# Performance work log

Hardware: AMD Instinct MI355X
Metric: run time of the kernel (lower is better)

The kernel has to match this reference:

```python
import jax, jax.numpy as jnp
import numpy as np

B, C, N = 8, 512, 2048

def setup_inputs() -> dict:
    key = jax.random.key(0)
    ks = jax.random.split(key, 7)
    s = 1.0 / np.sqrt(C)
    return {
        "x": jax.random.normal(ks[0], (B, C, N), dtype=jnp.float32),
        "wq": jax.random.normal(ks[1], (C, C), dtype=jnp.float32) * s,
        "bq": jax.random.normal(ks[2], (C,), dtype=jnp.float32) * s,
        "wk": jax.random.normal(ks[3], (C, C), dtype=jnp.float32) * s,
        "bk": jax.random.normal(ks[4], (C,), dtype=jnp.float32) * s,
        "wv": jax.random.normal(ks[5], (C, C), dtype=jnp.float32) * s,
        "bv": jax.random.normal(ks[6], (C,), dtype=jnp.float32) * s,
    }

def reference(x, wq, bq, wk, bk, wv, bv):
    # Conv1d with kernel=1 == pointwise channel matmul: [B,C,N] -> [B,C,N]
    q = jnp.einsum('oc,bcn->bon', wq, x) + bq[None, :, None]
    k = jnp.einsum('oc,bcn->bon', wk, x) + bk[None, :, None]
    v = jnp.einsum('oc,bcn->bon', wv, x) + bv[None, :, None]
    # scores[b,i,j] = sum_c q[b,c,i] * k[b,c,j]; softmax over j (no scaling, as in source)
    scores = jnp.einsum('bci,bcj->bij', q, k)
    attn = jax.nn.softmax(scores, axis=-1)  # [B,N,N]
    # out[b,c,i] = sum_j v[b,c,j] * attn[b,i,j]
    out = jnp.einsum('bcj,bij->bci', v, attn)
    return out + x
```

## Files before the change

kernel.cpp:

```cpp
#include <hip/hip_runtime.h>
#include <hip/hip_bf16.h>

typedef _Float16 half_t;
typedef _Float16 f16x8 __attribute__((ext_vector_type(8)));
typedef float f32x4 __attribute__((ext_vector_type(4)));

#define AS1 __attribute__((address_space(1)))
#define AS3 __attribute__((address_space(3)))

constexpr int CB = 512;
constexpr int NB = 2048;
constexpr int BB = 8;

__device__ inline f32x4 mfma16(f16x8 a, f16x8 b, f32x4 c) {
  return __builtin_amdgcn_mfma_f32_16x16x32_f16(a, b, c, 0, 0, 0);
}

__global__ void convert_w(const float* __restrict__ wv, half_t* __restrict__ wvh) {
  int i = blockIdx.x * 256 + threadIdx.x;
  if (i < CB * CB) wvh[i] = (half_t)wv[i];
}

__global__ __launch_bounds__(256) void compute_G_part(const float* __restrict__ wq,
                                                      const float* __restrict__ wk,
                                                      float* __restrict__ Gp) {
  __shared__ float aq[64][68];
  __shared__ float ak[64][68];
  const int c0 = blockIdx.y * 64, d0 = blockIdx.x * 64, o0 = blockIdx.z * 64;
  const int t = threadIdx.x;
  {
    const int r = t >> 2, cbase = (t & 3) * 16;
    const float* q = wq + (size_t)(o0 + r) * CB + c0 + cbase;
    const float* k = wk + (size_t)(o0 + r) * CB + d0 + cbase;
#pragma unroll
    for (int q4 = 0; q4 < 4; q4++) {
      *(float4*)&aq[r][cbase + q4 * 4] = *(const float4*)(q + q4 * 4);
      *(float4*)&ak[r][cbase + q4 * 4] = *(const float4*)(k + q4 * 4);
    }
  }
  __syncthreads();
  const int tc = t & 15, td = t >> 4;
  float acc[4][4] = {};
#pragma unroll 8
  for (int o = 0; o < 64; o++) {
    float4 a4 = *(const float4*)&aq[o][tc * 4];
    float4 b4 = *(const float4*)&ak[o][td * 4];
    float av[4] = {a4.x, a4.y, a4.z, a4.w};
    float bv[4] = {b4.x, b4.y, b4.z, b4.w};
#pragma unroll
    for (int i = 0; i < 4; i++)
#pragma unroll
      for (int j = 0; j < 4; j++)
        acc[i][j] += av[i] * bv[j];
  }
  float* gz = Gp + (size_t)blockIdx.z * CB * CB;
#pragma unroll
  for (int i = 0; i < 4; i++) {
    int c = c0 + tc * 4 + i;
#pragma unroll
    for (int j = 0; j < 4; j++)
      gz[(size_t)c * CB + d0 + td * 4 + j] = acc[i][j];
  }
}

__global__ void reduce_G(const float* __restrict__ Gp, half_t* __restrict__ Gh) {
  int i = blockIdx.x * 256 + threadIdx.x;
  if (i >= CB * CB) return;
  float s = 0.0f;
#pragma unroll
  for (int z = 0; z < 8; z++) s += Gp[(size_t)z * CB * CB + i];
  Gh[i] = (half_t)s;
}

__global__ void compute_u(const float* __restrict__ wk, const float* __restrict__ bq,
                          float* __restrict__ u) {
  int d = blockIdx.x * 256 + threadIdx.x;
  if (d >= CB) return;
  float s = 0.0f;
  for (int o = 0; o < CB; o++) s += bq[o] * wk[(size_t)o * CB + d];
  u[d] = s;
}

__global__ __launch_bounds__(256) void compute_ubias(const half_t* __restrict__ xh,
                                                     const float* __restrict__ u,
                                                     float* __restrict__ ub) {
  __shared__ float us[CB];
  for (int i = threadIdx.x; i < CB; i += 256) us[i] = u[i];
  __syncthreads();
  int row = blockIdx.x * 4 + (threadIdx.x >> 6);
  int lane = threadIdx.x & 63;
  f16x8 vh = *(const f16x8*)(xh + (size_t)row * CB + lane * 8);
  float s = 0.0f;
#pragma unroll
  for (int i = 0; i < 8; i++) s += us[lane * 8 + i] * (float)vh[i];
#pragma unroll
  for (int off = 32; off; off >>= 1) s += __shfl_xor(s, off);
  if (lane == 0) ub[row] = s;
}

__global__ void transpose_x(const float* __restrict__ x, half_t* __restrict__ oh,
                            half_t* __restrict__ xn) {
  __shared__ float tile[32][33];
  int b = blockIdx.z, c0 = blockIdx.y * 32, n0 = blockIdx.x * 32;
  int tx = threadIdx.x, ty = threadIdx.y;
  const float* xb = x + (size_t)b * CB * NB;
  half_t* xnb = xn + (size_t)b * CB * NB;
#pragma unroll
  for (int r = 0; r < 4; r++) {
    float v = xb[(size_t)(c0 + ty + 8 * r) * NB + n0 + tx];
    tile[ty + 8 * r][tx] = v;
    xnb[(size_t)(c0 + ty + 8 * r) * NB + n0 + tx] = (half_t)v;
  }
  __syncthreads();
  size_t base = (size_t)b * NB * CB;
#pragma unroll
  for (int r = 0; r < 4; r++)
    oh[base + (size_t)(n0 + ty + 8 * r) * CB + c0 + tx] = (half_t)tile[tx][ty + 8 * r];
}

template <int BIAS, int EPI, int BSPLIT>
__global__ __launch_bounds__(256) void gemm_nt(
    const half_t* __restrict__ A, int lda, long sA,
    const half_t* __restrict__ Bh, const half_t* __restrict__ Bl, int ldb, long sB,
    void* __restrict__ D, int ldd, long sD,
    const float* __restrict__ bias, long sBias,
    const half_t* __restrict__ R, int ldr, long sR,
    int K) {
  constexpr int PL = 2 + BSPLIT;
  constexpr int TSZ = 128 * 32;
  __shared__ alignas(16) half_t sm[2 * PL * TSZ];

  const int t = threadIdx.x;
  const int z = blockIdx.z;
  const half_t* Ab  = A  + (size_t)z * sA + (size_t)(blockIdx.y * 128) * lda;
  const half_t* Bbh = Bh + (size_t)z * sB + (size_t)(blockIdx.x * 128) * ldb;
  const half_t* Bbl = BSPLIT ? Bl + (size_t)z * sB + (size_t)(blockIdx.x * 128) * ldb : nullptr;
  const int wid = t >> 6, l15 = t & 15, hi = (t >> 4) & 3;
  const int wr = wid >> 1, wc = wid & 1;
  const int lineA = t >> 2, eoff = (t & 3) * 8;

  f32x4 acc[4][4] = {};

  auto stage = [&](int buf, int kt) {
    half_t* base = sm + buf * (PL * TSZ);
#pragma unroll
    for (int p = 0; p < 2; p++) {
      size_t goA = (size_t)(p * 64 + lineA) * lda + kt * 32 + eoff;
      size_t goB = (size_t)(p * 64 + lineA) * ldb + kt * 32 + eoff;
      int lo = p * 2048 + t * 8;
      __builtin_amdgcn_global_load_lds((const AS1 void*)(Ab + goA),  (AS3 void*)(base + lo), 16, 0, 0);
      __builtin_amdgcn_global_load_lds((const AS1 void*)(Bbh + goB), (AS3 void*)(base + TSZ + lo), 16, 0, 0);
      if (BSPLIT)
        __builtin_amdgcn_global_load_lds((const AS1 void*)(Bbl + goB), (AS3 void*)(base + 2 * TSZ + lo), 16, 0, 0);
    }
  };

  const int nt = K >> 5;
  stage(0, 0);
  __syncthreads();
  int cur = 0;
  for (int kt = 0; kt < nt; kt++) {
    if (kt + 1 < nt) stage(cur ^ 1, kt + 1);
    const half_t* bb = sm + cur * (PL * TSZ);
    f16x8 af[4], bfh[4], bfl[4];
#pragma unroll
    for (int f = 0; f < 4; f++) {
      int ao = (wr * 64 + f * 16 + l15) * 32 + hi * 8;
      int bo = (wc * 64 + f * 16 + l15) * 32 + hi * 8;
      af[f]  = *(const f16x8*)(bb + ao);
      bfh[f] = *(const f16x8*)(bb + TSZ + bo);
      if (BSPLIT) bfl[f] = *(const f16x8*)(bb + 2 * TSZ + bo);
    }
#pragma unroll
    for (int pass = 0; pass < 1 + BSPLIT; pass++) {
#pragma unroll
      for (int fm = 0; fm < 4; fm++)
#pragma unroll
        for (int fn = 0; fn < 4; fn++)
          acc[fm][fn] = mfma16(af[fm], (pass == 1) ? bfl[fn] : bfh[fn], acc[fm][fn]);
    }
    __syncthreads();
    cur ^= 1;
  }

  const int row0 = blockIdx.y * 128 + wr * 64;
  const int col0 = blockIdx.x * 128 + wc * 64;
#pragma unroll
  for (int fm = 0; fm < 4; fm++) {
    int rowb = row0 + fm * 16 + hi * 4;
#pragma unroll
    for (int fn = 0; fn < 4; fn++) {
      int col = col0 + fn * 16 + l15;
      float bc = (BIAS == 1) ? bias[(size_t)z * sBias + col] : 0.0f;
#pragma unroll
      for (int r = 0; r < 4; r++) {
        float val = acc[fm][fn][r] + bc;
        if (BIAS == 2) val += bias[(size_t)z * sBias + rowb + r];
        size_t di = (size_t)(rowb + r) * ldd + col;
        if (EPI == 0) {
          ((float*)D)[(size_t)z * sD + di] = val;
        } else if (EPI == 1) {
          ((half_t*)D)[(size_t)z * sD + di] = (half_t)val;
        } else if (EPI == 3) {
          val += (float)R[(size_t)z * sR + (size_t)(rowb + r) * ldr + col];
          ((float*)D)[(size_t)z * sD + di] = val;
        } else {
          float sv = fminf(fmaxf(val * 256.0f, -32767.0f), 32767.0f);
          ((short*)D)[(size_t)z * sD + di] = (short)__float2int_rn(sv);
        }
      }
    }
  }
}

struct alignas(16) H8 { half_t h[8]; };
struct alignas(16) S8 { short s[8]; };

__global__ __launch_bounds__(256) void softmax_rows(const short* __restrict__ S,
                                                    half_t* __restrict__ P) {
  const short* row = S + (size_t)blockIdx.x * NB;
  int t = threadIdx.x;
  S8 r8 = *reinterpret_cast<const S8*>(row + t * 8);
  float vals[8];
#pragma unroll
  for (int i = 0; i < 8; i++) vals[i] = (float)r8.s[i] * 0.00390625f;
  float m = vals[0];
#pragma unroll
  for (int i = 1; i < 8; i++) m = fmaxf(m, vals[i]);
#pragma unroll
  for (int off = 32; off; off >>= 1) m = fmaxf(m, __shfl_xor(m, off));
  __shared__ float redm[4], reds[4];
  if ((t & 63) == 0) redm[t >> 6] = m;
  __syncthreads();
  m = fmaxf(fmaxf(redm[0], redm[1]), fmaxf(redm[2], redm[3]));
  float e[8], s = 0.0f;
#pragma unroll
  for (int i = 0; i < 8; i++) { e[i] = __expf(vals[i] - m); s += e[i]; }
#pragma unroll
  for (int off = 32; off; off >>= 1) s += __shfl_xor(s, off);
  if ((t & 63) == 0) reds[t >> 6] = s;
  __syncthreads();
  s = reds[0] + reds[1] + reds[2] + reds[3];
  float inv = 1.0f / s;
  H8 ob;
#pragma unroll
  for (int i = 0; i < 8; i++) ob.h[i] = (half_t)(e[i] * inv);
  *reinterpret_cast<H8*>(P + (size_t)blockIdx.x * NB + t * 8) = ob;
}

extern "C" void kernel_launch(void* const* d_in, const int* in_sizes, int n_in,
                              void* d_out, int out_size, void* d_ws, size_t ws_size,
                              hipStream_t stream) {
  const float* x  = (const float*)d_in[0];
  const float* wq = (const float*)d_in[1];
  const float* bq = (const float*)d_in[2];
  const float* wk = (const float*)d_in[3];
  const float* wv = (const float*)d_in[5];
  const float* bv = (const float*)d_in[6];
  float* out = (float*)d_out;

  const size_t MB = 1u << 20;
  if (ws_size < 196 * MB) return;

  char* ws = (char*)d_ws;
  half_t* xh   = (half_t*)(ws + 0);
  half_t* YTh  = (half_t*)(ws + 16 * MB);
  half_t* v    = (half_t*)(ws + 32 * MB);
  short*  Ss   = (short*)(ws + 48 * MB);
  float*  Gp   = (float*)(ws + 48 * MB);
  half_t* Pd   = (half_t*)(ws + 112 * MB);
  half_t* xn   = (half_t*)(ws + 176 * MB);
  half_t* Gh   = (half_t*)(ws + 192 * MB);
  half_t* wvh  = (half_t*)(ws + 192 * MB + 512 * 1024);
  float*  u    = (float*)(ws + 193 * MB);
  float*  ub   = (float*)(ws + 193 * MB + 256 * 1024);

  convert_w<<<1024, 256, 0, stream>>>(wv, wvh);
  compute_G_part<<<dim3(8, 8, 8), 256, 0, stream>>>(wq, wk, Gp);
  reduce_G<<<1024, 256, 0, stream>>>(Gp, Gh);
  compute_u<<<2, 256, 0, stream>>>(wk, bq, u);
  transpose_x<<<dim3(64, 16, 8), dim3(32, 8), 0, stream>>>(x, xh, xn);
  compute_ubias<<<BB * NB / 4, 256, 0, stream>>>(xh, u, ub);

  gemm_nt<0, 1, 0><<<dim3(4, 16, 8), 256, 0, stream>>>(
      xh, CB, (long)NB * CB, Gh, nullptr, CB, 0,
      YTh, CB, (long)NB * CB, nullptr, 0, nullptr, 0, 0, CB);

  gemm_nt<2, 1, 0><<<dim3(16, 4, 8), 256, 0, stream>>>(
      wvh, CB, 0, xh, nullptr, CB, (long)NB * CB,
      v, NB, (long)CB * NB, bv, 0, nullptr, 0, 0, CB);

  gemm_nt<1, 4, 0><<<dim3(16, 16, 8), 256, 0, stream>>>(
      xh, CB, (long)NB * CB,
      YTh, nullptr, CB, (long)NB * CB,
      Ss, NB, (long)NB * NB, ub, NB, nullptr, 0, 0, CB);

  softmax_rows<<<BB * NB, 256, 0, stream>>>(Ss, Pd);

  gemm_nt<0, 3, 0><<<dim3(16, 4, 8), 256, 0, stream>>>(
      v, NB, (long)CB * NB,
      Pd, nullptr, NB, (long)NB * NB,
      out, NB, (long)CB * NB, nullptr, 0,
      xn, NB, (long)CB * NB, NB);
}
```

Baseline: 211.7 us.

## Merge V and YT projection GEMMs into one launch, add XCD block swizzle

Combines the two independent projection GEMMs (v = Wv·x + bv and YT = x·G) into a single kernel launch with a 16-deep z grid, so there is one launch and the GPU fills more CUs at once. Adds an XCD-aware block index remap to all GEMMs so neighbouring tiles land on the same chiplet for L2 reuse. Removes the unused BSPLIT path and dead epilogues. The swizzle could instead hurt locality for some grid shapes.

```diff
diff --git a/kernel.cpp b/kernel.cpp
--- a/kernel.cpp
+++ b/kernel.cpp
@@ -14,6 +14,20 @@
 
 __device__ inline f32x4 mfma16(f16x8 a, f16x8 b, f32x4 c) {
   return __builtin_amdgcn_mfma_f32_16x16x32_f16(a, b, c, 0, 0, 0);
+}
+
+__device__ inline void xcd_swizzle(int& bx, int& by, int& bz) {
+  const int gx = gridDim.x, gy = gridDim.y, gz = gridDim.z;
+  const int nwg = gx * gy * gz;
+  int lin = blockIdx.x + gx * (blockIdx.y + gy * blockIdx.z);
+  if ((nwg & 7) == 0) {
+    const int q = nwg >> 3;
+    lin = (lin & 7) * q + (lin >> 3);
+  }
+  bx = lin % gx;
+  int tmp = lin / gx;
+  by = tmp % gy;
+  bz = tmp / gy;
 }
 
 __global__ void convert_w(const float* __restrict__ wv, half_t* __restrict__ wvh) {
@@ -118,23 +132,23 @@
     oh[base + (size_t)(n0 + ty + 8 * r) * CB + c0 + tx] = (half_t)tile[tx][ty + 8 * r];
 }
 
-template <int BIAS, int EPI, int BSPLIT>
+template <int BIAS, int EPI>
 __global__ __launch_bounds__(256) void gemm_nt(
     const half_t* __restrict__ A, int lda, long sA,
-    const half_t* __restrict__ Bh, const half_t* __restrict__ Bl, int ldb, long sB,
+    const half_t* __restrict__ Bh, int ldb, long sB,
     void* __restrict__ D, int ldd, long sD,
     const float* __restrict__ bias, long sBias,
     const half_t* __restrict__ R, int ldr, long sR,
     int K) {
-  constexpr int PL = 2 + BSPLIT;
   constexpr int TSZ = 128 * 32;
-  __shared__ alignas(16) half_t sm[2 * PL * TSZ];
-
+  __shared__ alignas(16) half_t sm[2 * 2 * TSZ];
+
+  int bxi, byi, bzi;
+  xcd_swizzle(bxi, byi, bzi);
   const int t = threadIdx.x;
-  const int z = blockIdx.z;
-  const half_t* Ab  = A  + (size_t)z * sA + (size_t)(blockIdx.y * 128) * lda;
-  const half_t* Bbh = Bh + (size_t)z * sB + (size_t)(blockIdx.x * 128) * ldb;
-  const half_t* Bbl = BSPLIT ? Bl + (size_t)z * sB + (size_t)(blockIdx.x * 128) * ldb : nullptr;
+  const int z = bzi;
+  const half_t* Ab  = A  + (size_t)z * sA + (size_t)(byi * 128) * lda;
+  const half_t* Bbh = Bh + (size_t)z * sB + (size_t)(bxi * 128) * ldb;
   const int wid = t >> 6, l15 = t & 15, hi = (t >> 4) & 3;
   const int wr = wid >> 1, wc = wid & 1;
   const int lineA = t >> 2, eoff = (t & 3) * 8;
@@ -142,7 +156,7 @@
   f32x4 acc[4][4] = {};
 
   auto stage = [&](int buf, int kt) {
-    half_t* base = sm + buf * (PL * TSZ);
+    half_t* base = sm + buf * (2 * TSZ);
 #pragma unroll
     for (int p = 0; p < 2; p++) {
       size_t goA = (size_t)(p * 64 + lineA) * lda + kt * 32 + eoff;
@@ -150,8 +164,6 @@
       int lo = p * 2048 + t * 8;
       __builtin_amdgcn_global_load_lds((const AS1 void*)(Ab + goA),  (AS3 void*)(base + lo), 16, 0, 0);
       __builtin_amdgcn_global_load_lds((const AS1 void*)(Bbh + goB), (AS3 void*)(base + TSZ + lo), 16, 0, 0);
-      if (BSPLIT)
-        __builtin_amdgcn_global_load_lds((const AS1 void*)(Bbl + goB), (AS3 void*)(base + 2 * TSZ + lo), 16, 0, 0);
     }
   };
 
@@ -161,30 +173,24 @@
   int cur = 0;
   for (int kt = 0; kt < nt; kt++) {
     if (kt + 1 < nt) stage(cur ^ 1, kt + 1);
-    const half_t* bb = sm + cur * (PL * TSZ);
-    f16x8 af[4], bfh[4], bfl[4];
+    const half_t* bb = sm + cur * (2 * TSZ);
+    f16x8 af[4], bfh[4];
 #pragma unroll
     for (int f = 0; f < 4; f++) {
-      int ao = (wr * 64 + f * 16 + l15) * 32 + hi * 8;
-      int bo = (wc * 64 + f * 16 + l15) * 32 + hi * 8;
-      af[f]  = *(const f16x8*)(bb + ao);
-      bfh[f] = *(const f16x8*)(bb + TSZ + bo);
-      if (BSPLIT) bfl[f] = *(const f16x8*)(bb + 2 * TSZ + bo);
-    }
-#pragma unroll
-    for (int pass = 0; pass < 1 + BSPLIT; pass++) {
-#pragma unroll
-      for (int fm = 0; fm < 4; fm++)
-#pragma unroll
-        for (int fn = 0; fn < 4; fn++)
-          acc[fm][fn] = mfma16(af[fm], (pass == 1) ? bfl[fn] : bfh[fn], acc[fm][fn]);
-    }
+      af[f]  = *(const f16x8*)(bb + (wr * 64 + f * 16 + l15) * 32 + hi * 8);
+      bfh[f] = *(const f16x8*)(bb + TSZ + (wc * 64 + f * 16 + l15) * 32 + hi * 8);
+    }
+#pragma unroll
+    for (int fm = 0; fm < 4; fm++)
+#pragma unroll
+      for (int fn = 0; fn < 4; fn++)
+        acc[fm][fn] = mfma16(af[fm], bfh[fn], acc[fm][fn]);
     __syncthreads();
     cur ^= 1;
   }
 
-  const int row0 = blockIdx.y * 128 + wr * 64;
-  const int col0 = blockIdx.x * 128 + wc * 64;
+  const int row0 = byi * 128 + wr * 64;
+  const int col0 = bxi * 128 + wc * 64;
 #pragma unroll
   for (int fm = 0; fm < 4; fm++) {
     int rowb = row0 + fm * 16 + hi * 4;
@@ -195,19 +201,103 @@
 #pragma unroll
       for (int r = 0; r < 4; r++) {
         float val = acc[fm][fn][r] + bc;
-        if (BIAS == 2) val += bias[(size_t)z * sBias + rowb + r];
         size_t di = (size_t)(rowb + r) * ldd + col;
-        if (EPI == 0) {
-          ((float*)D)[(size_t)z * sD + di] = val;
-        } else if (EPI == 1) {
-          ((half_t*)D)[(size_t)z * sD + di] = (half_t)val;
-        } else if (EPI == 3) {
+        if (EPI == 3) {
           val += (float)R[(size_t)z * sR + (size_t)(rowb + r) * ldr + col];
           ((float*)D)[(size_t)z * sD + di] = val;
         } else {
           float sv = fminf(fmaxf(val * 256.0f, -32767.0f), 32767.0f);
           ((short*)D)[(size_t)z * sD + di] = (short)__float2int_rn(sv);
         }
+      }
+    }
+  }
+}
+
+__global__ __launch_bounds__(256) void gemm_vyt(
+    const half_t* __restrict__ xh, const half_t* __restrict__ wvh,
+    const half_t* __restrict__ Gh, const float* __restrict__ bv,
+    half_t* __restrict__ v, half_t* __restrict__ YTh) {
+  constexpr int TSZ = 128 * 32;
+  __shared__ alignas(16) half_t sm[2 * 2 * TSZ];
+
+  int bxi, byi, bzi;
+  xcd_swizzle(bxi, byi, bzi);
+  const int t = threadIdx.x;
+
+  const half_t* Ab;
+  const half_t* Bb;
+  half_t* Dz;
+  int ldd, row0b, col0b;
+  const float* rowbias = nullptr;
+  if (bzi < 8) {
+    const int z = bzi;
+    Ab = wvh + (size_t)(byi * 128) * CB;
+    Bb = xh + (size_t)z * NB * CB + (size_t)(bxi * 128) * CB;
+    Dz = v + (size_t)z * CB * NB;
+    ldd = NB; row0b = byi * 128; col0b = bxi * 128;
+    rowbias = bv;
+  } else {
+    const int z = bzi - 8;
+    const int lin2 = byi * 16 + bxi;
+    const int xp = lin2 & 3, yp = lin2 >> 2;
+    Ab = xh + (size_t)z * NB * CB + (size_t)(yp * 128) * CB;
+    Bb = Gh + (size_t)(xp * 128) * CB;
+    Dz = YTh + (size_t)z * NB * CB;
+    ldd = CB; row0b = yp * 128; col0b = xp * 128;
+  }
+
+  const int wid = t >> 6, l15 = t & 15, hi = (t >> 4) & 3;
+  const int wr = wid >> 1, wc = wid & 1;
+  const int lineA = t >> 2, eoff = (t & 3) * 8;
+
+  f32x4 acc[4][4] = {};
+
+  auto stage = [&](int buf, int kt) {
+    half_t* base = sm + buf * (2 * TSZ);
+#pragma unroll
+    for (int p = 0; p < 2; p++) {
+      size_t go = (size_t)(p * 64 + lineA) * CB + kt * 32 + eoff;
+      int lo = p * 2048 + t * 8;
+      __builtin_amdgcn_global_load_lds((const AS1 void*)(Ab + go), (AS3 void*)(base + lo), 16, 0, 0);
+      __builtin_amdgcn_global_load_lds((const AS1 void*)(Bb + go), (AS3 void*)(base + TSZ + lo), 16, 0, 0);
+    }
+  };
+
+  stage(0, 0);
+  __syncthreads();
+  int cur = 0;
+  for (int kt = 0; kt < 16; kt++) {
+    if (kt + 1 < 16) stage(cur ^ 1, kt + 1);
+    const half_t* bb = sm + cur * (2 * TSZ);
+    f16x8 af[4], bf[4];
+#pragma unroll
+    for (int f = 0; f < 4; f++) {
+      af[f] = *(const f16x8*)(bb + (wr * 64 + f * 16 + l15) * 32 + hi * 8);
+      bf[f] = *(const f16x8*)(bb + TSZ + (wc * 64 + f * 16 + l15) * 32 + hi * 8);
+    }
+#pragma unroll
+    for (int fm = 0; fm < 4; fm++)
+#pragma unroll
+      for (int fn = 0; fn < 4; fn++)
+        acc[fm][fn] = mfma16(af[fm], bf[fn], acc[fm][fn]);
+    __syncthreads();
+    cur ^= 1;
+  }
+
+  const int row0 = row0b + wr * 64;
+  const int col0 = col0b + wc * 64;
+#pragma unroll
+  for (int fm = 0; fm < 4; fm++) {
+    int rowb = row0 + fm * 16 + hi * 4;
+#pragma unroll
+    for (int fn = 0; fn < 4; fn++) {
+      int col = col0 + fn * 16 + l15;
+#pragma unroll
+      for (int r = 0; r < 4; r++) {
+        float val = acc[fm][fn][r];
+        if (rowbias) val += rowbias[rowb + r];
+        Dz[(size_t)(rowb + r) * ldd + col] = (half_t)val;
       }
     }
   }
@@ -282,24 +372,18 @@
   transpose_x<<<dim3(64, 16, 8), dim3(32, 8), 0, stream>>>(x, xh, xn);
   compute_ubias<<<BB * NB / 4, 256, 0, stream>>>(xh, u, ub);
 
-  gemm_nt<0, 1, 0><<<dim3(4, 16, 8), 256, 0, stream>>>(
-      xh, CB, (long)NB * CB, Gh, nullptr, CB, 0,
-      YTh, CB, (long)NB * CB, nullptr, 0, nullptr, 0, 0, CB);
-
-  gemm_nt<2, 1, 0><<<dim3(16, 4, 8), 256, 0, stream>>>(
-      wvh, CB, 0, xh, nullptr, CB, (long)NB * CB,
-      v, NB, (long)CB * NB, bv, 0, nullptr, 0, 0, CB);
-
-  gemm_nt<1, 4, 0><<<dim3(16, 16, 8), 256, 0, stream>>>(
+  gemm_vyt<<<dim3(16, 4, 16), 256, 0, stream>>>(xh, wvh, Gh, bv, v, YTh);
+
+  gemm_nt<1, 4><<<dim3(16, 16, 8), 256, 0, stream>>>(
       xh, CB, (long)NB * CB,
-      YTh, nullptr, CB, (long)NB * CB,
+      YTh, CB, (long)NB * CB,
       Ss, NB, (long)NB * NB, ub, NB, nullptr, 0, 0, CB);
 
   softmax_rows<<<BB * NB, 256, 0, stream>>>(Ss, Pd);
 
-  gemm_nt<0, 3, 0><<<dim3(16, 4, 8), 256, 0, stream>>>(
+  gemm_nt<0, 3><<<dim3(16, 4, 8), 256, 0, stream>>>(
       v, NB, (long)CB * NB,
-      Pd, nullptr, NB, (long)NB * NB,
+      Pd, NB, (long)NB * NB,
       out, NB, (long)CB * NB, nullptr, 0,
       xn, NB, (long)CB * NB, NB);
 }
```

After: 203.1 us. 1.04x faster.
